# Kernel optimization log

Measured on AMD Instinct MI355X. Metric: run time of the kernel, lower is better.

The kernel has to match this reference:

```python
import jax, jax.numpy as jnp
import numpy as np
from jax import lax

ORDER = 6
SAMPLES = 64
TOPK = 512
STRIDE = 2          # contour features are stride-2 w.r.t. input ('1' level)
NMS_THRESH = 0.2
REF_ITERS = 4
REF_MARGIN = 3.0
HC = WC = 256       # contour-feature grid
HF = WF = 512       # full-res (refinement) grid


def conv2d(x, w, b=None, pad=0):
    # x: [B,C,H,W], w: [O,I,kh,kw]
    y = lax.conv_general_dilated(x, w, (1, 1), [(pad, pad), (pad, pad)],
                                 dimension_numbers=("NCHW", "OIHW", "NCHW"))
    if b is not None:
        y = y + b[None, :, None, None]
    return y


def setup_inputs() -> dict:
    key = jax.random.key(0)
    ks = jax.random.split(key, 16)
    s = 0.05
    d = {
        "contour_features": jax.random.normal(ks[0], (4, 64, HC, WC), jnp.float32),
        "enc_score_features": jax.random.normal(ks[1], (4, 64, HC, WC), jnp.float32),
        "refinement_features": jax.random.normal(ks[2], (4, 32, HF, WF), jnp.float32),
        "enc_refinement_features": jax.random.normal(ks[3], (4, 32, HF, WF), jnp.float32),
        # learned params
        "w_score_reduce": jax.random.normal(ks[4], (64, 128, 1, 1)) * s,
        "w_score": jax.random.normal(ks[5], (2, 64, 7, 7)) * s,
        "b_score": jnp.zeros((2,), jnp.float32),
        "w_loc": jax.random.normal(ks[6], (2, 64, 7, 7)) * s,
        "b_loc": jnp.zeros((2,), jnp.float32),
        "w_fourier": jax.random.normal(ks[7], (ORDER * 4, 64, 7, 7)) * s,
        "b_fourier": jnp.zeros((ORDER * 4,), jnp.float32),
        "w_ref_reduce": jax.random.normal(ks[8], (32, 64, 1, 1)) * s,
        "w_ref": jax.random.normal(ks[9], (2, 32, 7, 7)) * s,
        "b_ref": jnp.zeros((2,), jnp.float32),
    }
    return d


def _pairwise_iou(boxes):
    # boxes: [K,4] as (x1,y1,x2,y2)
    x1, y1, x2, y2 = boxes[:, 0], boxes[:, 1], boxes[:, 2], boxes[:, 3]
    area = jnp.maximum(x2 - x1, 0.) * jnp.maximum(y2 - y1, 0.)
    ix1 = jnp.maximum(x1[:, None], x1[None, :])
    iy1 = jnp.maximum(y1[:, None], y1[None, :])
    ix2 = jnp.minimum(x2[:, None], x2[None, :])
    iy2 = jnp.minimum(y2[:, None], y2[None, :])
    inter = jnp.maximum(ix2 - ix1, 0.) * jnp.maximum(iy2 - iy1, 0.)
    union = area[:, None] + area[None, :] - inter
    return inter / jnp.maximum(union, 1e-8)


def _nms_keep(boxes, valid):
    # boxes sorted by descending score. Sequential greedy NMS.
    iou = _pairwise_iou(boxes)  # [K,K]
    idx = jnp.arange(TOPK)

    def body(i, keep):
        sup = (iou[i] > NMS_THRESH) & keep[i] & (idx > i)
        return keep & ~sup

    keep = lax.fori_loop(0, TOPK, body, valid)
    return keep


def _forward(contour_features, enc_score_features, refinement_features,
             enc_refinement_features, w_score_reduce, w_score, b_score,
             w_loc, b_loc, w_fourier, b_fourier, w_ref_reduce, w_ref, b_ref):
    B = contour_features.shape[0]
    # ---- dense heads (CPNCore.forward) ----
    sf = conv2d(jnp.concatenate([contour_features, enc_score_features], 1), w_score_reduce)
    score_logits = conv2d(sf, w_score, b_score, pad=3)            # [B,2,HC,WC]
    log_scores = jax.nn.log_softmax(score_logits, axis=1)
    locations = conv2d(contour_features, w_loc, b_loc, pad=3)     # [B,2,HC,WC]
    fourier = conv2d(contour_features, w_fourier, b_fourier, pad=3)  # [B,4*ORDER,HC,WC]

    rf = conv2d(jnp.concatenate([refinement_features, enc_refinement_features], 1), w_ref_reduce)
    refinement = jnp.tanh(conv2d(rf, w_ref, b_ref, pad=3)) * REF_MARGIN  # [B,2,HF,WF]

    # ---- proposal selection: top-K foreground scores ----
    fg = jnp.exp(log_scores[:, 1])                                # [B,HC,WC]
    fg_flat = fg.reshape(B, -1)
    top_scores, top_idx = lax.top_k(fg_flat, TOPK)                # [B,K] sorted desc
    valid = top_scores > 0.5                                      # score_thresh

    gy = (top_idx // WC).astype(jnp.float32)
    gx = (top_idx % WC).astype(jnp.float32)

    def gather_ch(t):  # t: [B,C,HC,WC] -> [B,K,C]
        C = t.shape[1]
        tf = t.reshape(B, C, -1)
        out = jnp.take_along_axis(tf, top_idx[:, None, :].repeat(C, axis=1), axis=2)
        return out.transpose(0, 2, 1)

    loc = gather_ch(locations)                                    # [B,K,2] (x,y offsets)
    fr = gather_ch(fourier).reshape(B, TOPK, ORDER, 4)            # a_x,b_x,a_y,b_y

    cx = (gx + loc[..., 0]) * STRIDE
    cy = (gy + loc[..., 1]) * STRIDE

    # ---- fourier -> contour sampling ----
    t = jnp.arange(SAMPLES, dtype=jnp.float32) / SAMPLES
    k = jnp.arange(1, ORDER + 1, dtype=jnp.float32)
    ang = 2.0 * jnp.pi * k[:, None] * t[None, :]                  # [ORDER,SAMPLES]
    cos, sin = jnp.cos(ang), jnp.sin(ang)
    px = jnp.einsum('bko,os->bks', fr[..., 0], cos) + jnp.einsum('bko,os->bks', fr[..., 1], sin)
    py = jnp.einsum('bko,os->bks', fr[..., 2], cos) + jnp.einsum('bko,os->bks', fr[..., 3], sin)
    contour = jnp.stack([px * STRIDE + cx[..., None], py * STRIDE + cy[..., None]], -1)  # [B,K,S,2]

    # ---- iterative local refinement (nearest-neighbor gather) ----
    ref_flat = refinement.reshape(B, 2, -1)
    for _ in range(REF_ITERS):
        xi = jnp.clip(jnp.round(contour[..., 0]), 0, WF - 1).astype(jnp.int32)
        yi = jnp.clip(jnp.round(contour[..., 1]), 0, HF - 1).astype(jnp.int32)
        flat = (yi * WF + xi).reshape(B, 1, -1)                   # [B,1,K*S]
        off = jnp.take_along_axis(ref_flat, flat.repeat(2, axis=1), axis=2)
        off = off.reshape(B, 2, TOPK, SAMPLES).transpose(0, 2, 3, 1)  # [B,K,S,2]
        contour = contour + off

    # ---- boxes + NMS ----
    boxes = jnp.concatenate([contour.min(axis=2), contour.max(axis=2)], -1)  # [B,K,4]
    keep = jax.vmap(_nms_keep)(boxes, valid)
    return contour, top_scores, keep, boxes


def reference(contour_features, enc_score_features, refinement_features,
              enc_refinement_features, w_score_reduce, w_score, b_score,
              w_loc, b_loc, w_fourier, b_fourier, w_ref_reduce, w_ref, b_ref):
    return _forward(contour_features, enc_score_features, refinement_features,
                    enc_refinement_features, w_score_reduce, w_score, b_score,
                    w_loc, b_loc, w_fourier, b_fourier, w_ref_reduce, w_ref, b_ref)
```

## Files before the change

kernel.cpp:

```cpp
#include <hip/hip_runtime.h>
#include <math.h>

#define WS_FG    0ull
#define WS_REF   3145728ull
#define WS_PART  11534336ull
#define WS_WSE   19922944ull
#define WS_WRE   20023296ull
#define WS_WG    20073472ull
#define WS_TIDX  20399616ull
#define WS_GATH  20407808ull
#define WS_TRIG  20620800ull
#define WS_END   20899328ull

__global__ __launch_bounds__(256) void cpn_prep_kernel(
    const float* __restrict__ w_score_reduce, const float* __restrict__ w_score,
    const float* __restrict__ w_loc, const float* __restrict__ w_fourier,
    const float* __restrict__ w_ref_reduce, const float* __restrict__ w_ref,
    double* __restrict__ wse, double* __restrict__ wre, float* __restrict__ wg,
    float* __restrict__ trig)
{
    int i = blockIdx.x * 256 + threadIdx.x;
    if (i < 12544) {
        int o = i / 6272;
        int rem = i % 6272;
        int c = rem / 49, r = rem % 49;
        double a = 0.0;
        for (int m = 0; m < 64; ++m)
            a += (double)w_score[(o*64 + m)*49 + r] * (double)w_score_reduce[m*128 + c];
        wse[i] = a;
    } else if (i < 12544 + 6272) {
        int t = i - 12544;
        int o = t / 3136;
        int rem = t % 3136;
        int c = rem / 49, r = rem % 49;
        double a = 0.0;
        for (int m = 0; m < 32; ++m)
            a += (double)w_ref[(o*32 + m)*49 + r] * (double)w_ref_reduce[m*64 + c];
        wre[t] = a;
    } else if (i < 12544 + 6272 + 81536) {
        int t = i - 18816;
        int tap = t / 26, o = t % 26;
        wg[t] = (o < 2) ? w_loc[o*3136 + tap] : w_fourier[(o - 2)*3136 + tap];
    } else if (i < 100352 + 768) {
        int t = i - 100352;
        int cs = t / 384;
        int k = (t % 384) / 64, s = t % 64;
        const float TWO_PI_F = (float)6.283185307179586;
        float a1 = TWO_PI_F * (float)(k + 1);
        float tf = (float)s * 0.015625f;
        float ang = a1 * tf;
        double av = (double)ang;
        trig[t] = (cs == 0) ? (float)cos(av) : (float)sin(av);
    }
}

__global__ __launch_bounds__(256) void cpn_score_conv_kernel(
    const float* __restrict__ cf, const float* __restrict__ esf,
    const double* __restrict__ wse, double2* __restrict__ partial)
{
    __shared__ __align__(16) double wch[32][7][14];
    __shared__ __align__(16) float patch[38*44];
    const int tid  = threadIdx.x;
    const int b    = blockIdx.z >> 1;
    const int half = blockIdx.z & 1;
    const int c0   = half * 64;
    const float* src = half ? esf : cf;
    const int row0 = blockIdx.y * 32;
    const int col0 = blockIdx.x * 32;
    const int ty   = tid >> 3;
    const int txg  = tid & 7;

    double acc0[4] = {0.0,0.0,0.0,0.0};
    double acc1[4] = {0.0,0.0,0.0,0.0};
    float sreg[6];

    {
        const float* sp = src + (size_t)(b*64) * 65536;
        #pragma unroll
        for (int k = 0; k < 6; ++k) {
            int i = k*256 + tid; float v = 0.f;
            if (i < 1520) {
                int r = i/40, j = i%40;
                int gy = row0 - 3 + r, gx = col0 - 4 + j;
                if ((unsigned)gy < 256u && (unsigned)gx < 256u) v = sp[gy*256 + gx];
            }
            sreg[k] = v;
        }
    }

    for (int c = 0; c < 64; ++c) {
        if ((c & 31) == 0) {
            for (int i = tid; i < 32*98; i += 256) {
                int cc = i / 98, r = i % 98;
                int ky = r / 14, q = r % 14;
                int kx = q >> 1, o = q & 1;
                wch[cc][ky][q] = wse[o*6272 + (c0 + c + cc)*49 + ky*7 + kx];
            }
        }
        #pragma unroll
        for (int k = 0; k < 6; ++k) {
            int i = k*256 + tid;
            if (i < 1520) patch[(i/40)*44 + (i%40)] = sreg[k];
        }
        __syncthreads();
        if (c + 1 < 64) {
            const float* sp = src + (size_t)(b*64 + (c+1)) * 65536;
            #pragma unroll
            for (int k = 0; k < 6; ++k) {
                int i = k*256 + tid; float v = 0.f;
                if (i < 1520) {
                    int r = i/40, j = i%40;
                    int gy = row0 - 3 + r, gx = col0 - 4 + j;
                    if ((unsigned)gy < 256u && (unsigned)gx < 256u) v = sp[gy*256 + gx];
                }
                sreg[k] = v;
            }
        }
        const int cl = c & 31;
        #pragma unroll
        for (int ky = 0; ky < 7; ++ky) {
            const float4* pr = reinterpret_cast<const float4*>(&patch[(ty+ky)*44 + txg*4]);
            float4 A = pr[0], B2 = pr[1], C2 = pr[2];
            float rv[12] = {A.x,A.y,A.z,A.w,B2.x,B2.y,B2.z,B2.w,C2.x,C2.y,C2.z,C2.w};
            const double* wp = &wch[cl][ky][0];
            #pragma unroll
            for (int kx = 0; kx < 7; ++kx) {
                double w0 = wp[2*kx], w1 = wp[2*kx+1];
                #pragma unroll
                for (int p = 0; p < 4; ++p) {
                    double v = (double)rv[p + kx + 1];
                    acc0[p] = fma(w0, v, acc0[p]);
                    acc1[p] = fma(w1, v, acc1[p]);
                }
            }
        }
        __syncthreads();
    }

    int y = row0 + ty;
    #pragma unroll
    for (int p = 0; p < 4; ++p) {
        int x = col0 + txg*4 + p;
        double2 v; v.x = acc0[p]; v.y = acc1[p];
        partial[(size_t)(half*4 + b)*65536 + y*256 + x] = v;
    }
}

__global__ __launch_bounds__(256) void cpn_score_fin_kernel(
    const double2* __restrict__ partial, const float* __restrict__ b_score,
    float* __restrict__ fg)
{
    int i = blockIdx.x * 256 + threadIdx.x;
    int b = i >> 16, px = i & 65535;
    double2 p0 = partial[(size_t)b*65536 + px];
    double2 p1 = partial[(size_t)(4 + b)*65536 + px];
    double bs0 = (double)b_score[0], bs1 = (double)b_score[1];
    float l0f = (float)((p0.x + p1.x) + bs0);
    float l1f = (float)((p0.y + p1.y) + bs1);
    float m  = fmaxf(l0f, l1f);
    float e0 = (float)exp((double)(l0f - m));
    float e1 = (float)exp((double)(l1f - m));
    float s  = e0 + e1;
    float lg = (float)log((double)s);
    float ls1 = (l1f - m) - lg;
    float fgv = (float)exp((double)ls1);
    fg[i] = fgv;
}

__global__ __launch_bounds__(256) void cpn_ref_conv_kernel(
    const float* __restrict__ rff, const float* __restrict__ erf,
    const double* __restrict__ wre, const float* __restrict__ b_ref,
    float* __restrict__ refmap)
{
    __shared__ __align__(16) float4 patch4[38][19];
    __shared__ __align__(16) float wlds[64][7][14];
    const int tid  = threadIdx.x;
    const int b    = blockIdx.z;
    const int row0 = blockIdx.y * 32;
    const int col0 = blockIdx.x * 64;
    const int tyg  = tid & 31;
    const int txg  = tid >> 5;

    for (int i = tid; i < 64*98; i += 256) {
        int c = i / 98, r = i % 98;
        int ky = r / 14, q = r % 14;
        int kx = q >> 1, o = q & 1;
        wlds[c][ky][q] = (float)wre[o*3136 + c*49 + ky*7 + kx];
    }

    int   st_r[3], st_f[3];
    long  st_off[3];
    bool  st_ok[3];
    #pragma unroll
    for (int k = 0; k < 3; ++k) {
        int i = k*256 + tid;
        int r = i / 18, f = i % 18;
        int gy = row0 - 3 + r, gx = col0 - 4 + 4*f;
        st_r[k] = r; st_f[k] = f;
        st_ok[k] = (i < 684) && ((unsigned)gy < 512u) && ((unsigned)gx < 509u);
        st_off[k] = (long)gy * 512 + gx;
    }

    float4 s4[3];
    {
        const float* sp = rff + (size_t)(b*32) * 262144;
        #pragma unroll
        for (int k = 0; k < 3; ++k) {
            float4 v = {0.f,0.f,0.f,0.f};
            if (st_ok[k]) v = *reinterpret_cast<const float4*>(sp + st_off[k]);
            s4[k] = v;
        }
    }

    float acc0[8] = {0,0,0,0,0,0,0,0};
    float acc1[8] = {0,0,0,0,0,0,0,0};

    for (int c = 0; c < 64; ++c) {
        #pragma unroll
        for (int k = 0; k < 3; ++k) {
            int i = k*256 + tid;
            if (i < 684) patch4[st_r[k]][st_f[k]] = s4[k];
        }
        __syncthreads();
        if (c + 1 < 64) {
            int cn = c + 1;
            const float* src = (cn < 32) ? rff : erf;
            const float* sp = src + (size_t)(b*32 + (cn & 31)) * 262144;
            #pragma unroll
            for (int k = 0; k < 3; ++k) {
                float4 v = {0.f,0.f,0.f,0.f};
                if (st_ok[k]) v = *reinterpret_cast<const float4*>(sp + st_off[k]);
                s4[k] = v;
            }
        }
        #pragma unroll
        for (int pr = 0; pr < 7; ++pr) {
            int row = tyg + pr;
            float4 A = patch4[row][2*txg + 0];
            float4 B2 = patch4[row][2*txg + 1];
            float4 C2 = patch4[row][2*txg + 2];
            float4 D2 = patch4[row][2*txg + 3];
            float rv[16] = {A.x,A.y,A.z,A.w,B2.x,B2.y,B2.z,B2.w,
                            C2.x,C2.y,C2.z,C2.w,D2.x,D2.y,D2.z,D2.w};
            const float* wp = &wlds[c][pr][0];
            float wv[14];
            #pragma unroll
            for (int q = 0; q < 14; ++q) wv[q] = wp[q];
            #pragma unroll
            for (int kx = 0; kx < 7; ++kx) {
                float w0 = wv[2*kx], w1 = wv[2*kx+1];
                #pragma unroll
                for (int p = 0; p < 8; ++p) {
                    float v = rv[p + kx + 1];
                    acc0[p] = fmaf(w0, v, acc0[p]);
                    acc1[p] = fmaf(w1, v, acc1[p]);
                }
            }
        }
        __syncthreads();
    }

    float br0 = b_ref[0], br1 = b_ref[1];
    int y = row0 + tyg;
    int x0 = col0 + txg*8;
    #pragma unroll
    for (int p = 0; p < 8; ++p) {
        float t0 = tanhf(acc0[p] + br0);
        float t1 = tanhf(acc1[p] + br1);
        refmap[((size_t)(b*2 + 0)*512 + y)*512 + x0 + p] = t0 * 3.0f;
        refmap[((size_t)(b*2 + 1)*512 + y)*512 + x0 + p] = t1 * 3.0f;
    }
}

__device__ __forceinline__ void cpn_find_bucket(
    unsigned int* hist, unsigned int* seg, int nb, int target, int tid,
    int* s_bsel, int* s_cnt)
{
    int nseg = nb / 32;
    for (int t = tid; t < nseg; t += 1024) {
        unsigned int s = 0;
        for (int q = 0; q < 32; ++q) s += hist[t*32 + q];
        seg[t] = s;
    }
    __syncthreads();
    if (tid == 0) {
        int cum = 0, sg = 0;
        for (int jj = nseg - 1; jj >= 0; --jj) {
            int c = (int)seg[jj];
            if (cum + c >= target) { sg = jj; break; }
            cum += c;
        }
        int bs = sg*32;
        for (int jj = sg*32 + 31; jj >= sg*32; --jj) {
            int c = (int)hist[jj];
            if (cum + c >= target) { bs = jj; break; }
            cum += c;
        }
        *s_bsel = bs; *s_cnt = cum;
    }
    __syncthreads();
}

__global__ __launch_bounds__(1024) void cpn_topk_kernel(
    const float* __restrict__ fg, int* __restrict__ tidx, float* __restrict__ tscores)
{
    const int b = blockIdx.x;
    const int tid = threadIdx.x;
    const float* f = fg + (size_t)b * 65536;

    __shared__ unsigned int hist[2048];
    __shared__ unsigned int seg[64];
    __shared__ int tie[2048];
    __shared__ int sel_idx[512];
    __shared__ unsigned int skey[512];
    __shared__ int sidx[512];
    __shared__ int s_b, s_c, s_nsel, s_ntie;

    const int bitsA[3]  = {11,11,10};
    const int shiftA[3] = {21,10,0};

    unsigned int prefix = 0;
    int target = 512;
    for (int pass = 0; pass < 3; ++pass) {
        int sh = shiftA[pass], nb = 1 << bitsA[pass];
        for (int i = tid; i < 2048; i += 1024) hist[i] = 0;
        __syncthreads();
        if (pass == 0) {
            for (int i = tid; i < 65536; i += 1024) {
                unsigned int k = __float_as_uint(f[i]);
                atomicAdd(&hist[k >> 21], 1u);
            }
        } else {
            int hs = sh + bitsA[pass];
            for (int i = tid; i < 65536; i += 1024) {
                unsigned int k = __float_as_uint(f[i]);
                if ((k >> hs) == prefix)
                    atomicAdd(&hist[(k >> sh) & (nb-1)], 1u);
            }
        }
        __syncthreads();
        cpn_find_bucket(hist, seg, nb, target, tid, &s_b, &s_c);
        prefix = (prefix << bitsA[pass]) | (unsigned)s_b;
        target -= s_c;
    }
    if (tid == 0) { s_nsel = 0; s_ntie = 0; }
    __syncthreads();
    const unsigned int K = prefix;

    for (int i = tid; i < 65536; i += 1024) {
        unsigned int k = __float_as_uint(f[i]);
        if (k > K) { int q = atomicAdd(&s_nsel, 1); sel_idx[q] = i; }
        else if (k == K) { int q = atomicAdd(&s_ntie, 1); if (q < 2048) tie[q] = i; }
    }
    __syncthreads();
    int nsel = s_nsel;
    int nt = s_ntie; if (nt > 2048) nt = 2048;
    for (int q = tid; q < 2048; q += 1024) if (q >= nt) tie[q] = 0x7FFFFFFF;
    __syncthreads();

    for (int kk = 2; kk <= 2048; kk <<= 1)
        for (int jj = kk >> 1; jj > 0; jj >>= 1) {
            for (int i = tid; i < 2048; i += 1024) {
                int ixj = i ^ jj;
                if (ixj > i) {
                    int a = tie[i], c = tie[ixj];
                    bool up = ((i & kk) == 0);
                    if (up ? (a > c) : (a < c)) { tie[i] = c; tie[ixj] = a; }
                }
            }
            __syncthreads();
        }

    for (int q = tid; q < 512; q += 1024) {
        unsigned int k2; int i2;
        if (q < nsel) { i2 = sel_idx[q]; k2 = __float_as_uint(f[i2]); }
        else          { i2 = tie[q - nsel]; k2 = K; }
        skey[q] = k2; sidx[q] = i2;
    }
    __syncthreads();
    for (int kk = 2; kk <= 512; kk <<= 1)
        for (int jj = kk >> 1; jj > 0; jj >>= 1) {
            if (tid < 512) {
                int i = tid, ixj = i ^ jj;
                if (ixj > i) {
                    unsigned int ka = skey[i], kc = skey[ixj];
                    int ia = sidx[i], ic = sidx[ixj];
                    bool up = ((i & kk) == 0);
                    bool aBefore = (ka > kc) || (ka == kc && ia < ic);
                    if (up ? !aBefore : aBefore) {
                        skey[i] = kc; skey[ixj] = ka;
                        sidx[i] = ic; sidx[ixj] = ia;
                    }
                }
            }
            __syncthreads();
        }
    for (int q = tid; q < 512; q += 1024) {
        int i2 = sidx[q];
        tscores[b*512 + q] = f[i2];
        tidx[b*512 + q] = i2;
    }
}

__global__ __launch_bounds__(256) void cpn_gather_conv_kernel(
    const float* __restrict__ cf, const float* __restrict__ wg,
    const float* __restrict__ b_loc, const float* __restrict__ b_fourier,
    const int* __restrict__ tidx, float* __restrict__ gath)
{
    const int b = blockIdx.y, p = blockIdx.x, tid = threadIdx.x;
    const int idx = tidx[b*512 + p];
    const int gy = idx >> 8, gx = idx & 255;

    double part[26];
    #pragma unroll
    for (int o = 0; o < 26; ++o) part[o] = 0.0;

    for (int t = tid; t < 3136; t += 256) {
        int c = t / 49, rr = t % 49, ky = rr / 7, kx = rr % 7;
        int y = gy + ky - 3, x = gx + kx - 3;
        float v = 0.f;
        if ((unsigned)y < 256u && (unsigned)x < 256u)
            v = cf[((size_t)(b*64 + c)*256 + y)*256 + x];
        const float* wr = wg + t*26;
        double dv = (double)v;
        #pragma unroll
        for (int o = 0; o < 26; ++o) part[o] = fma(dv, (double)wr[o], part[o]);
    }
    #pragma unroll
    for (int o = 0; o < 26; ++o)
        for (int off = 32; off; off >>= 1) part[o] += __shfl_down(part[o], off, 64);

    __shared__ double red[4][26];
    int w = tid >> 6, lane = tid & 63;
    if (lane == 0) {
        #pragma unroll
        for (int o = 0; o < 26; ++o) red[w][o] = part[o];
    }
    __syncthreads();
    if (tid < 26) {
        double s = red[0][tid] + red[1][tid] + red[2][tid] + red[3][tid];
        s += (tid < 2) ? (double)b_loc[tid] : (double)b_fourier[tid - 2];
        gath[((size_t)b*512 + p)*26 + tid] = (float)s;
    }
}

__global__ __launch_bounds__(64) void cpn_contour_kernel(
    const float* __restrict__ gath, const int* __restrict__ tidx,
    const float* __restrict__ refmap, const float* __restrict__ trig,
    float* __restrict__ out_contour, float* __restrict__ out_boxes)
{
    const int bp = blockIdx.x;
    const int b = bp >> 9;
    const int s = threadIdx.x;
    const float* g = gath + (size_t)bp * 26;
    const int idx = tidx[bp];
    const int gy = idx >> 8, gx = idx & 255;

    float cx = ((float)gx + g[0]) * 2.0f;
    float cy = ((float)gy + g[1]) * 2.0f;

    float sxc = 0.f, sxs = 0.f, syc = 0.f, sys = 0.f;
    #pragma unroll
    for (int k = 0; k < 6; ++k) {
        float cs = trig[k*64 + s];
        float sn = trig[384 + k*64 + s];
        float t0 = g[2 + k*4 + 0] * cs; asm volatile("" : "+v"(t0)); sxc += t0;
        float t1 = g[2 + k*4 + 1] * sn; asm volatile("" : "+v"(t1)); sxs += t1;
        float t2 = g[2 + k*4 + 2] * cs; asm volatile("" : "+v"(t2)); syc += t2;
        float t3 = g[2 + k*4 + 3] * sn; asm volatile("" : "+v"(t3)); sys += t3;
    }
    float px = sxc + sxs;
    float py = syc + sys;
    float x = px * 2.0f; asm volatile("" : "+v"(x)); x += cx;
    float y = py * 2.0f; asm volatile("" : "+v"(y)); y += cy;

    const float* r0 = refmap + (size_t)b * 2 * 262144;
    const float* r1 = r0 + 262144;
    #pragma unroll
    for (int it = 0; it < 4; ++it) {
        float xr = rintf(x); xr = fminf(fmaxf(xr, 0.f), 511.f);
        float yr = rintf(y); yr = fminf(fmaxf(yr, 0.f), 511.f);
        int xi = (int)xr, yi = (int)yr;
        x += r0[yi*512 + xi];
        y += r1[yi*512 + xi];
    }

    out_contour[((size_t)bp*64 + s)*2 + 0] = x;
    out_contour[((size_t)bp*64 + s)*2 + 1] = y;

    float mnx = x, mxx = x, mny = y, mxy = y;
    #pragma unroll
    for (int off = 32; off; off >>= 1) {
        mnx = fminf(mnx, __shfl_xor(mnx, off, 64));
        mny = fminf(mny, __shfl_xor(mny, off, 64));
        mxx = fmaxf(mxx, __shfl_xor(mxx, off, 64));
        mxy = fmaxf(mxy, __shfl_xor(mxy, off, 64));
    }
    if (s == 0) {
        out_boxes[bp*4 + 0] = mnx;
        out_boxes[bp*4 + 1] = mny;
        out_boxes[bp*4 + 2] = mxx;
        out_boxes[bp*4 + 3] = mxy;
    }
}

__global__ __launch_bounds__(512) void cpn_nms_kernel(
    const float* __restrict__ boxes, const float* __restrict__ scores,
    float* __restrict__ keep_out)
{
    const int b = blockIdx.x;
    const int j = threadIdx.x;
    __shared__ float X1[512], Y1[512], X2[512], Y2[512], AR[512];
    __shared__ int keep[512];

    const float* bb = boxes + b*512*4;
    float x1 = bb[j*4+0], y1 = bb[j*4+1], x2 = bb[j*4+2], y2 = bb[j*4+3];
    float aj = fmaxf(x2 - x1, 0.f) * fmaxf(y2 - y1, 0.f);
    X1[j] = x1; Y1[j] = y1; X2[j] = x2; Y2[j] = y2; AR[j] = aj;
    keep[j] = (scores[b*512 + j] > 0.5f) ? 1 : 0;
    __syncthreads();

    for (int i = 0; i < 512; ++i) {
        if (keep[i] && j > i) {
            float ix1 = fmaxf(x1, X1[i]);
            float iy1 = fmaxf(y1, Y1[i]);
            float ix2 = fminf(x2, X2[i]);
            float iy2 = fminf(y2, Y2[i]);
            float inter = fmaxf(ix2 - ix1, 0.f) * fmaxf(iy2 - iy1, 0.f);
            float uni = (aj + AR[i]) - inter;
            float iou = inter / fmaxf(uni, 1e-8f);
            if (iou > 0.2f) keep[j] = 0;
        }
        __syncthreads();
    }
    keep_out[b*512 + j] = keep[j] ? 1.0f : 0.0f;
}

extern "C" void kernel_launch(void* const* d_in, const int* in_sizes, int n_in,
                              void* d_out, int out_size, void* d_ws, size_t ws_size,
                              hipStream_t stream)
{
    if (ws_size < WS_END) return;

    const float* cf   = (const float*)d_in[0];
    const float* esf  = (const float*)d_in[1];
    const float* rff  = (const float*)d_in[2];
    const float* erf  = (const float*)d_in[3];
    const float* w_sr = (const float*)d_in[4];
    const float* w_s  = (const float*)d_in[5];
    const float* b_s  = (const float*)d_in[6];
    const float* w_l  = (const float*)d_in[7];
    const float* b_l  = (const float*)d_in[8];
    const float* w_f  = (const float*)d_in[9];
    const float* b_f  = (const float*)d_in[10];
    const float* w_rr = (const float*)d_in[11];
    const float* w_r  = (const float*)d_in[12];
    const float* b_r  = (const float*)d_in[13];

    char* ws = (char*)d_ws;
    float*   fg   = (float*)(ws + WS_FG);
    float*   refm = (float*)(ws + WS_REF);
    double2* part = (double2*)(ws + WS_PART);
    double*  wse  = (double*)(ws + WS_WSE);
    double*  wre  = (double*)(ws + WS_WRE);
    float*   wg   = (float*)(ws + WS_WG);
    int*     tidx = (int*)(ws + WS_TIDX);
    float*   gath = (float*)(ws + WS_GATH);
    float*   trig = (float*)(ws + WS_TRIG);

    float* out_contour = (float*)d_out;
    float* out_scores  = out_contour + 262144;
    float* out_keep    = out_scores + 2048;
    float* out_boxes   = out_keep + 2048;

    cpn_prep_kernel<<<dim3(395), dim3(256), 0, stream>>>(
        w_sr, w_s, w_l, w_f, w_rr, w_r, wse, wre, wg, trig);
    cpn_score_conv_kernel<<<dim3(8, 8, 8), dim3(256), 0, stream>>>(
        cf, esf, wse, part);
    cpn_ref_conv_kernel<<<dim3(8, 16, 4), dim3(256), 0, stream>>>(
        rff, erf, wre, b_r, refm);
    cpn_score_fin_kernel<<<dim3(1024), dim3(256), 0, stream>>>(
        part, b_s, fg);
    cpn_topk_kernel<<<dim3(4), dim3(1024), 0, stream>>>(fg, tidx, out_scores);
    cpn_gather_conv_kernel<<<dim3(512, 4), dim3(256), 0, stream>>>(
        cf, wg, b_l, b_f, tidx, gath);
    cpn_contour_kernel<<<dim3(2048), dim3(64), 0, stream>>>(
        gath, tidx, refm, trig, out_contour, out_boxes);
    cpn_nms_kernel<<<dim3(4), dim3(512), 0, stream>>>(
        out_boxes, out_scores, out_keep);
}
```

Before: 724.1 us.

## Run score conv in fp32, reselect top-k candidates with exact fp64 recompute

```diff
diff --git a/kernel.cpp b/kernel.cpp
--- a/kernel.cpp
+++ b/kernel.cpp
@@ -1,16 +1,19 @@
 #include <hip/hip_runtime.h>
 #include <math.h>
 
-#define WS_FG    0ull
-#define WS_REF   3145728ull
-#define WS_PART  11534336ull
-#define WS_WSE   19922944ull
-#define WS_WRE   20023296ull
-#define WS_WG    20073472ull
-#define WS_TIDX  20399616ull
-#define WS_GATH  20407808ull
-#define WS_TRIG  20620800ull
-#define WS_END   20899328ull
+#define WS_D     0ull
+#define WS_REF   1048576ull
+#define WS_SPART 9437184ull
+#define WS_WSE   13631488ull
+#define WS_WRE   13731840ull
+#define WS_WG    13782016ull
+#define WS_TIDX  14108160ull
+#define WS_GATH  14116352ull
+#define WS_TRIG  14329344ull
+#define WS_CLIST 14332416ull
+#define WS_CNT   14365184ull
+#define WS_PAIRS 14365200ull
+#define WS_END   14430736ull
 
 __global__ __launch_bounds__(256) void cpn_prep_kernel(
     const float* __restrict__ w_score_reduce, const float* __restrict__ w_score,
@@ -54,11 +57,11 @@
     }
 }
 
-__global__ __launch_bounds__(256) void cpn_score_conv_kernel(
+__global__ __launch_bounds__(256) void cpn_score_dense_kernel(
     const float* __restrict__ cf, const float* __restrict__ esf,
-    const double* __restrict__ wse, double2* __restrict__ partial)
-{
-    __shared__ __align__(16) double wch[32][7][14];
+    const double* __restrict__ wse, float2* __restrict__ partial)
+{
+    __shared__ __align__(16) float wch[32][7][14];
     __shared__ __align__(16) float patch[38*44];
     const int tid  = threadIdx.x;
     const int b    = blockIdx.z >> 1;
@@ -70,8 +73,8 @@
     const int ty   = tid >> 3;
     const int txg  = tid & 7;
 
-    double acc0[4] = {0.0,0.0,0.0,0.0};
-    double acc1[4] = {0.0,0.0,0.0,0.0};
+    float acc0[4] = {0.f,0.f,0.f,0.f};
+    float acc1[4] = {0.f,0.f,0.f,0.f};
     float sreg[6];
 
     {
@@ -94,7 +97,7 @@
                 int cc = i / 98, r = i % 98;
                 int ky = r / 14, q = r % 14;
                 int kx = q >> 1, o = q & 1;
-                wch[cc][ky][q] = wse[o*6272 + (c0 + c + cc)*49 + ky*7 + kx];
+                wch[cc][ky][q] = (float)wse[o*6272 + (c0 + c + cc)*49 + ky*7 + kx];
             }
         }
         #pragma unroll
@@ -122,15 +125,18 @@
             const float4* pr = reinterpret_cast<const float4*>(&patch[(ty+ky)*44 + txg*4]);
             float4 A = pr[0], B2 = pr[1], C2 = pr[2];
             float rv[12] = {A.x,A.y,A.z,A.w,B2.x,B2.y,B2.z,B2.w,C2.x,C2.y,C2.z,C2.w};
-            const double* wp = &wch[cl][ky][0];
+            const float* wp = &wch[cl][ky][0];
+            float wv[14];
+            #pragma unroll
+            for (int q = 0; q < 14; ++q) wv[q] = wp[q];
             #pragma unroll
             for (int kx = 0; kx < 7; ++kx) {
-                double w0 = wp[2*kx], w1 = wp[2*kx+1];
+                float w0 = wv[2*kx], w1 = wv[2*kx+1];
                 #pragma unroll
                 for (int p = 0; p < 4; ++p) {
-                    double v = (double)rv[p + kx + 1];
-                    acc0[p] = fma(w0, v, acc0[p]);
-                    acc1[p] = fma(w1, v, acc1[p]);
+                    float v = rv[p + kx + 1];
+                    acc0[p] = fmaf(w0, v, acc0[p]);
+                    acc1[p] = fmaf(w1, v, acc1[p]);
                 }
             }
         }
@@ -141,30 +147,21 @@
     #pragma unroll
     for (int p = 0; p < 4; ++p) {
         int x = col0 + txg*4 + p;
-        double2 v; v.x = acc0[p]; v.y = acc1[p];
+        float2 v; v.x = acc0[p]; v.y = acc1[p];
         partial[(size_t)(half*4 + b)*65536 + y*256 + x] = v;
     }
 }
 
-__global__ __launch_bounds__(256) void cpn_score_fin_kernel(
-    const double2* __restrict__ partial, const float* __restrict__ b_score,
-    float* __restrict__ fg)
+__global__ __launch_bounds__(256) void cpn_dcomb_kernel(
+    const float2* __restrict__ partial, float* __restrict__ d)
 {
     int i = blockIdx.x * 256 + threadIdx.x;
     int b = i >> 16, px = i & 65535;
-    double2 p0 = partial[(size_t)b*65536 + px];
-    double2 p1 = partial[(size_t)(4 + b)*65536 + px];
-    double bs0 = (double)b_score[0], bs1 = (double)b_score[1];
-    float l0f = (float)((p0.x + p1.x) + bs0);
-    float l1f = (float)((p0.y + p1.y) + bs1);
-    float m  = fmaxf(l0f, l1f);
-    float e0 = (float)exp((double)(l0f - m));
-    float e1 = (float)exp((double)(l1f - m));
-    float s  = e0 + e1;
-    float lg = (float)log((double)s);
-    float ls1 = (l1f - m) - lg;
-    float fgv = (float)exp((double)ls1);
-    fg[i] = fgv;
+    float2 p0 = partial[(size_t)b*65536 + px];
+    float2 p1 = partial[(size_t)(4 + b)*65536 + px];
+    float l0 = p0.x + p1.x;
+    float l1 = p0.y + p1.y;
+    d[i] = l1 - l0;
 }
 
 __global__ __launch_bounds__(256) void cpn_ref_conv_kernel(
@@ -172,7 +169,6 @@
     const double* __restrict__ wre, const float* __restrict__ b_ref,
     float* __restrict__ refmap)
 {
-    __shared__ __align__(16) float4 patch4[38][19];
     __shared__ __align__(16) float wlds[64][7][14];
     const int tid  = threadIdx.x;
     const int b    = blockIdx.z;
@@ -187,59 +183,32 @@
         int kx = q >> 1, o = q & 1;
         wlds[c][ky][q] = (float)wre[o*3136 + c*49 + ky*7 + kx];
     }
-
-    int   st_r[3], st_f[3];
-    long  st_off[3];
-    bool  st_ok[3];
-    #pragma unroll
-    for (int k = 0; k < 3; ++k) {
-        int i = k*256 + tid;
-        int r = i / 18, f = i % 18;
-        int gy = row0 - 3 + r, gx = col0 - 4 + 4*f;
-        st_r[k] = r; st_f[k] = f;
-        st_ok[k] = (i < 684) && ((unsigned)gy < 512u) && ((unsigned)gx < 509u);
-        st_off[k] = (long)gy * 512 + gx;
-    }
-
-    float4 s4[3];
-    {
-        const float* sp = rff + (size_t)(b*32) * 262144;
-        #pragma unroll
-        for (int k = 0; k < 3; ++k) {
-            float4 v = {0.f,0.f,0.f,0.f};
-            if (st_ok[k]) v = *reinterpret_cast<const float4*>(sp + st_off[k]);
-            s4[k] = v;
-        }
-    }
+    __syncthreads();
+
+    const int gx0 = col0 + txg*8 - 4;
+    bool cok[4];
+    #pragma unroll
+    for (int f = 0; f < 4; ++f) {
+        int g = gx0 + 4*f;
+        cok[f] = (g >= 0) && (g + 3 <= 511);
+    }
+    const int ybase = row0 + tyg - 3;
 
     float acc0[8] = {0,0,0,0,0,0,0,0};
     float acc1[8] = {0,0,0,0,0,0,0,0};
 
     for (int c = 0; c < 64; ++c) {
-        #pragma unroll
-        for (int k = 0; k < 3; ++k) {
-            int i = k*256 + tid;
-            if (i < 684) patch4[st_r[k]][st_f[k]] = s4[k];
-        }
-        __syncthreads();
-        if (c + 1 < 64) {
-            int cn = c + 1;
-            const float* src = (cn < 32) ? rff : erf;
-            const float* sp = src + (size_t)(b*32 + (cn & 31)) * 262144;
-            #pragma unroll
-            for (int k = 0; k < 3; ++k) {
-                float4 v = {0.f,0.f,0.f,0.f};
-                if (st_ok[k]) v = *reinterpret_cast<const float4*>(sp + st_off[k]);
-                s4[k] = v;
-            }
-        }
+        const float* sp = ((c < 32) ? rff : erf) + ((size_t)(b*32 + (c & 31)) << 18);
         #pragma unroll
         for (int pr = 0; pr < 7; ++pr) {
-            int row = tyg + pr;
-            float4 A = patch4[row][2*txg + 0];
-            float4 B2 = patch4[row][2*txg + 1];
-            float4 C2 = patch4[row][2*txg + 2];
-            float4 D2 = patch4[row][2*txg + 3];
+            int gy = ybase + pr;
+            bool rok = ((unsigned)gy < 512u);
+            const float* rp = sp + gy*512 + gx0;
+            float4 A  = {0,0,0,0}, B2 = {0,0,0,0}, C2 = {0,0,0,0}, D2 = {0,0,0,0};
+            if (rok && cok[0]) A  = *reinterpret_cast<const float4*>(rp);
+            if (rok && cok[1]) B2 = *reinterpret_cast<const float4*>(rp + 4);
+            if (rok && cok[2]) C2 = *reinterpret_cast<const float4*>(rp + 8);
+            if (rok && cok[3]) D2 = *reinterpret_cast<const float4*>(rp + 12);
             float rv[16] = {A.x,A.y,A.z,A.w,B2.x,B2.y,B2.z,B2.w,
                             C2.x,C2.y,C2.z,C2.w,D2.x,D2.y,D2.z,D2.w};
             const float* wp = &wlds[c][pr][0];
@@ -257,7 +226,6 @@
                 }
             }
         }
-        __syncthreads();
     }
 
     float br0 = b_ref[0], br1 = b_ref[1];
@@ -301,20 +269,21 @@
     __syncthreads();
 }
 
-__global__ __launch_bounds__(1024) void cpn_topk_kernel(
-    const float* __restrict__ fg, int* __restrict__ tidx, float* __restrict__ tscores)
+__device__ __forceinline__ unsigned int cpn_fkey(float v) {
+    unsigned int u = __float_as_uint(v);
+    return (u & 0x80000000u) ? ~u : (u | 0x80000000u);
+}
+
+__global__ __launch_bounds__(1024) void cpn_select_kernel(
+    const float* __restrict__ d, int* __restrict__ clist, int* __restrict__ cnt)
 {
     const int b = blockIdx.x;
     const int tid = threadIdx.x;
-    const float* f = fg + (size_t)b * 65536;
+    const float* f = d + (size_t)b * 65536;
 
     __shared__ unsigned int hist[2048];
     __shared__ unsigned int seg[64];
-    __shared__ int tie[2048];
-    __shared__ int sel_idx[512];
-    __shared__ unsigned int skey[512];
-    __shared__ int sidx[512];
-    __shared__ int s_b, s_c, s_nsel, s_ntie;
+    __shared__ int s_b, s_c, s_n;
 
     const int bitsA[3]  = {11,11,10};
     const int shiftA[3] = {21,10,0};
@@ -327,13 +296,13 @@
         __syncthreads();
         if (pass == 0) {
             for (int i = tid; i < 65536; i += 1024) {
-                unsigned int k = __float_as_uint(f[i]);
+                unsigned int k = cpn_fkey(f[i]);
                 atomicAdd(&hist[k >> 21], 1u);
             }
         } else {
             int hs = sh + bitsA[pass];
             for (int i = tid; i < 65536; i += 1024) {
-                unsigned int k = __float_as_uint(f[i]);
+                unsigned int k = cpn_fkey(f[i]);
                 if ((k >> hs) == prefix)
                     atomicAdd(&hist[(k >> sh) & (nb-1)], 1u);
             }
@@ -343,52 +312,101 @@
         prefix = (prefix << bitsA[pass]) | (unsigned)s_b;
         target -= s_c;
     }
-    if (tid == 0) { s_nsel = 0; s_ntie = 0; }
-    __syncthreads();
-    const unsigned int K = prefix;
-
+    float T = (prefix & 0x80000000u) ? __uint_as_float(prefix & 0x7FFFFFFFu)
+                                     : __uint_as_float(~prefix);
+    float tval = T - 0.0625f;
+
+    if (tid == 0) s_n = 0;
+    __syncthreads();
     for (int i = tid; i < 65536; i += 1024) {
-        unsigned int k = __float_as_uint(f[i]);
-        if (k > K) { int q = atomicAdd(&s_nsel, 1); sel_idx[q] = i; }
-        else if (k == K) { int q = atomicAdd(&s_ntie, 1); if (q < 2048) tie[q] = i; }
-    }
-    __syncthreads();
-    int nsel = s_nsel;
-    int nt = s_ntie; if (nt > 2048) nt = 2048;
-    for (int q = tid; q < 2048; q += 1024) if (q >= nt) tie[q] = 0x7FFFFFFF;
-    __syncthreads();
-
+        if (f[i] >= tval) {
+            int q = atomicAdd(&s_n, 1);
+            if (q < 2048) clist[b*2048 + q] = i;
+        }
+    }
+    __syncthreads();
+    if (tid == 0) cnt[b] = (s_n > 2048) ? 2048 : s_n;
+}
+
+__global__ __launch_bounds__(256) void cpn_recompute_kernel(
+    const float* __restrict__ cf, const float* __restrict__ esf,
+    const double* __restrict__ wse, const float* __restrict__ b_score,
+    const int* __restrict__ clist, const int* __restrict__ cnt,
+    uint2* __restrict__ pairs)
+{
+    const int b = blockIdx.y, q = blockIdx.x, tid = threadIdx.x;
+    const int n = cnt[b];
+    if (q >= n) {
+        if (tid == 0) { uint2 pd; pd.x = 0u; pd.y = 0x7FFFFFFFu; pairs[b*2048 + q] = pd; }
+        return;
+    }
+    const int idx = clist[b*2048 + q];
+    const int gy = idx >> 8, gx = idx & 255;
+
+    double L0 = 0.0, L1 = 0.0;
+    for (int t = tid; t < 6272; t += 256) {
+        int c = t / 49, r = t % 49, ky = r / 7, kx = r % 7;
+        int y = gy + ky - 3, x = gx + kx - 3;
+        float v = 0.f;
+        if ((unsigned)y < 256u && (unsigned)x < 256u) {
+            const float* src = (c < 64) ? cf : esf;
+            v = src[((size_t)(b*64 + (c & 63)) << 16) + y*256 + x];
+        }
+        double dv = (double)v;
+        L0 = fma(dv, wse[c*49 + r], L0);
+        L1 = fma(dv, wse[6272 + c*49 + r], L1);
+    }
+    #pragma unroll
+    for (int off = 32; off; off >>= 1) {
+        L0 += __shfl_down(L0, off, 64);
+        L1 += __shfl_down(L1, off, 64);
+    }
+    __shared__ double red[4][2];
+    int w = tid >> 6, lane = tid & 63;
+    if (lane == 0) { red[w][0] = L0; red[w][1] = L1; }
+    __syncthreads();
+    if (tid == 0) {
+        double S0 = red[0][0] + red[1][0] + red[2][0] + red[3][0];
+        double S1 = red[0][1] + red[1][1] + red[2][1] + red[3][1];
+        float l0f = (float)(S0 + (double)b_score[0]);
+        float l1f = (float)(S1 + (double)b_score[1]);
+        float m  = fmaxf(l0f, l1f);
+        float e0 = (float)exp((double)(l0f - m));
+        float e1 = (float)exp((double)(l1f - m));
+        float s  = e0 + e1;
+        float lg = (float)log((double)s);
+        float ls1 = (l1f - m) - lg;
+        float fgv = (float)exp((double)ls1);
+        uint2 pr; pr.x = __float_as_uint(fgv); pr.y = (unsigned)idx;
+        pairs[b*2048 + q] = pr;
+    }
+}
+
+__global__ __launch_bounds__(1024) void cpn_sortk_kernel(
+    const uint2* __restrict__ pairs, int* __restrict__ tidx,
+    float* __restrict__ tscores)
+{
+    const int b = blockIdx.x;
+    const int tid = threadIdx.x;
+    __shared__ unsigned int key[2048];
+    __shared__ int sidx[2048];
+
+    for (int q = tid; q < 2048; q += 1024) {
+        uint2 pr = pairs[b*2048 + q];
+        key[q] = pr.x; sidx[q] = (int)pr.y;
+    }
+    __syncthreads();
     for (int kk = 2; kk <= 2048; kk <<= 1)
         for (int jj = kk >> 1; jj > 0; jj >>= 1) {
             for (int i = tid; i < 2048; i += 1024) {
                 int ixj = i ^ jj;
                 if (ixj > i) {
-                    int a = tie[i], c = tie[ixj];
-                    bool up = ((i & kk) == 0);
-                    if (up ? (a > c) : (a < c)) { tie[i] = c; tie[ixj] = a; }
-                }
-            }
-            __syncthreads();
-        }
-
-    for (int q = tid; q < 512; q += 1024) {
-        unsigned int k2; int i2;
-        if (q < nsel) { i2 = sel_idx[q]; k2 = __float_as_uint(f[i2]); }
-        else          { i2 = tie[q - nsel]; k2 = K; }
-        skey[q] = k2; sidx[q] = i2;
-    }
-    __syncthreads();
-    for (int kk = 2; kk <= 512; kk <<= 1)
-        for (int jj = kk >> 1; jj > 0; jj >>= 1) {
-            if (tid < 512) {
-                int i = tid, ixj = i ^ jj;
-                if (ixj > i) {
-                    unsigned int ka = skey[i], kc = skey[ixj];
+                    unsigned int ka = key[i], kc = key[ixj];
                     int ia = sidx[i], ic = sidx[ixj];
                     bool up = ((i & kk) == 0);
                     bool aBefore = (ka > kc) || (ka == kc && ia < ic);
                     if (up ? !aBefore : aBefore) {
-                        skey[i] = kc; skey[ixj] = ka;
+                        key[i] = kc; key[ixj] = ka;
                         sidx[i] = ic; sidx[ixj] = ia;
                     }
                 }
@@ -396,9 +414,8 @@
             __syncthreads();
         }
     for (int q = tid; q < 512; q += 1024) {
-        int i2 = sidx[q];
-        tscores[b*512 + q] = f[i2];
-        tidx[b*512 + q] = i2;
+        tscores[b*512 + q] = __uint_as_float(key[q]);
+        tidx[b*512 + q] = sidx[q];
     }
 }
 
@@ -558,15 +575,18 @@
     const float* b_r  = (const float*)d_in[13];
 
     char* ws = (char*)d_ws;
-    float*   fg   = (float*)(ws + WS_FG);
-    float*   refm = (float*)(ws + WS_REF);
-    double2* part = (double2*)(ws + WS_PART);
-    double*  wse  = (double*)(ws + WS_WSE);
-    double*  wre  = (double*)(ws + WS_WRE);
-    float*   wg   = (float*)(ws + WS_WG);
-    int*     tidx = (int*)(ws + WS_TIDX);
-    float*   gath = (float*)(ws + WS_GATH);
-    float*   trig = (float*)(ws + WS_TRIG);
+    float*  dbuf = (float*)(ws + WS_D);
+    float*  refm = (float*)(ws + WS_REF);
+    float2* spart = (float2*)(ws + WS_SPART);
+    double* wse  = (double*)(ws + WS_WSE);
+    double* wre  = (double*)(ws + WS_WRE);
+    float*  wg   = (float*)(ws + WS_WG);
+    int*    tidx = (int*)(ws + WS_TIDX);
+    float*  gath = (float*)(ws + WS_GATH);
+    float*  trig = (float*)(ws + WS_TRIG);
+    int*    clist = (int*)(ws + WS_CLIST);
+    int*    cnt  = (int*)(ws + WS_CNT);
+    uint2*  pairs = (uint2*)(ws + WS_PAIRS);
 
     float* out_contour = (float*)d_out;
     float* out_scores  = out_contour + 262144;
@@ -575,13 +595,15 @@
 
     cpn_prep_kernel<<<dim3(395), dim3(256), 0, stream>>>(
         w_sr, w_s, w_l, w_f, w_rr, w_r, wse, wre, wg, trig);
-    cpn_score_conv_kernel<<<dim3(8, 8, 8), dim3(256), 0, stream>>>(
-        cf, esf, wse, part);
+    cpn_score_dense_kernel<<<dim3(8, 8, 8), dim3(256), 0, stream>>>(
+        cf, esf, wse, spart);
     cpn_ref_conv_kernel<<<dim3(8, 16, 4), dim3(256), 0, stream>>>(
         rff, erf, wre, b_r, refm);
-    cpn_score_fin_kernel<<<dim3(1024), dim3(256), 0, stream>>>(
-        part, b_s, fg);
-    cpn_topk_kernel<<<dim3(4), dim3(1024), 0, stream>>>(fg, tidx, out_scores);
+    cpn_dcomb_kernel<<<dim3(1024), dim3(256), 0, stream>>>(spart, dbuf);
+    cpn_select_kernel<<<dim3(4), dim3(1024), 0, stream>>>(dbuf, clist, cnt);
+    cpn_recompute_kernel<<<dim3(2048, 4), dim3(256), 0, stream>>>(
+        cf, esf, wse, b_s, clist, cnt, pairs);
+    cpn_sortk_kernel<<<dim3(4), dim3(1024), 0, stream>>>(pairs, tidx, out_scores);
     cpn_gather_conv_kernel<<<dim3(512, 4), dim3(256), 0, stream>>>(
         cf, wg, b_l, b_f, tidx, gath);
     cpn_contour_kernel<<<dim3(2048), dim3(64), 0, stream>>>(
```

Result: slower. 1.227 ms (+69.5%).
